# Performance work log

Measured on AMD Instinct MI355X. Metric: run time of the kernel, lower is better.

Reference implementation:

```python
import jax, jax.numpy as jnp
import numpy as np

COST_CLASS = 1.0
COST_MASK = 5.0
COST_DICE = 5.0


def _sample_points(masks, coords):
    """Bilinear grid_sample (align_corners=False, zero padding).

    masks:  [N, H, W] float
    coords: [P, 2] in [0, 1], (x, y) order as in torch grid_sample
    returns [N, P]
    """
    H, W = masks.shape[-2], masks.shape[-1]
    # torch: grid = 2*c - 1; pixel = ((grid+1)*size - 1)/2 = c*size - 0.5
    x = coords[:, 0] * W - 0.5
    y = coords[:, 1] * H - 0.5
    x0 = jnp.floor(x)
    y0 = jnp.floor(y)
    tx = (x - x0).astype(masks.dtype)
    ty = (y - y0).astype(masks.dtype)
    x0i = x0.astype(jnp.int32)
    y0i = y0.astype(jnp.int32)

    def gather(ix, iy):
        valid = ((ix >= 0) & (ix < W) & (iy >= 0) & (iy < H)).astype(masks.dtype)
        v = masks[:, jnp.clip(iy, 0, H - 1), jnp.clip(ix, 0, W - 1)]  # [N, P]
        return v * valid

    v00 = gather(x0i, y0i)
    v01 = gather(x0i + 1, y0i)
    v10 = gather(x0i, y0i + 1)
    v11 = gather(x0i + 1, y0i + 1)
    return (v00 * (1 - tx) * (1 - ty) + v01 * tx * (1 - ty)
            + v10 * (1 - tx) * ty + v11 * tx * ty)


def _cost_one(pred_mask, pred_logits, tgt_mask, labels, coords):
    # pred_mask [Q,H,W], pred_logits [Q,C], tgt_mask [T,H,W], labels [T], coords [P,2]
    probs = jax.nn.softmax(pred_logits, axis=-1)          # [Q, C]
    cost_class = -probs[:, labels]                        # [Q, T]

    pm = _sample_points(pred_mask, coords)                # [Q, P] logits
    tm = _sample_points(tgt_mask, coords)                 # [T, P] in [0,1]
    P = pm.shape[1]

    # pair-wise sigmoid BCE: BCE(x, 1) = softplus(-x), BCE(x, 0) = softplus(x)
    ce_pos = jax.nn.softplus(-pm) / P                     # [Q, P]
    ce_neg = jax.nn.softplus(pm) / P                      # [Q, P]
    cost_mask = ce_pos @ tm.T + ce_neg @ (1.0 - tm).T     # [Q, T]

    # pair-wise dice
    sig = jax.nn.sigmoid(pm)                              # [Q, P]
    numerator = 2.0 * (sig @ tm.T)                        # [Q, T]
    denominator = sig.sum(-1)[:, None] + tm.sum(-1)[None, :]
    cost_dice = 1.0 - (numerator + 1.0) / (denominator + 1.0)

    return COST_MASK * cost_mask + COST_CLASS * cost_class + COST_DICE * cost_dice


def setup_inputs() -> dict:
    key = jax.random.key(0)
    k1, k2, k3, k4, k5 = jax.random.split(key, 5)
    B, Q, C, T, H, W, P = 8, 150, 134, 32, 160, 160, 12544
    masks_queries_logits = jax.random.normal(k1, (B, Q, H, W), dtype=jnp.float32)
    class_queries_logits = jax.random.normal(k2, (B, Q, C), dtype=jnp.float32)
    # binary target masks
    mask_labels = (jax.random.uniform(k3, (B, T, H, W)) > 0.5).astype(jnp.float32)
    class_labels = jax.random.randint(k4, (B, T), 0, 133, dtype=jnp.int64)
    point_coords = jax.random.uniform(k5, (B, P, 2), dtype=jnp.float32)
    return {
        "masks_queries_logits": masks_queries_logits,
        "class_queries_logits": class_queries_logits,
        "mask_labels": mask_labels,
        "class_labels": class_labels,
        "point_coords": point_coords,
    }


def reference(masks_queries_logits, class_queries_logits, mask_labels, class_labels, point_coords):
    # Returns the per-sample cost matrices [B, Q, T] (the GPU-side work of the
    # matcher). The scipy Hungarian assignment on these matrices is CPU-bound
    # and intentionally excluded from the kernel baseline.
    cost = jax.vmap(_cost_one)(
        masks_queries_logits, class_queries_logits, mask_labels, class_labels, point_coords
    )
    return cost
```

## Files before the change

### kernel.cpp

```cpp
#include <hip/hip_runtime.h>
#include <hip/hip_bf16.h>
#include <hip/hip_fp16.h>
#include <math.h>

#define B_ 8
#define Q_ 150
#define QP_ 160
#define C_ 134
#define T_ 32
#define H_ 160
#define W_ 160
#define P_ 12544
#define HW_ (H_ * W_)
#define HW4_ (HW_ / 4)

#define SBLK 1024
#define SFULL 12
#define STAIL 256
#define SEG_ 28
#define KSEG 448
#define KITER 14
#define DSTRIDE (2 * B_ * QP_ * T_)

typedef __attribute__((ext_vector_type(8))) short short8;
typedef __attribute__((ext_vector_type(4))) float floatx4;

struct Samp {
  int i00, i01, i10, i11;
  float w00, w01, w10, w11;
};

__device__ __forceinline__ Samp make_samp(float cx, float cy) {
  float x = cx * (float)W_ - 0.5f;
  float y = cy * (float)H_ - 0.5f;
  float x0f = floorf(x), y0f = floorf(y);
  float tx = x - x0f, ty = y - y0f;
  int x0 = (int)x0f, y0 = (int)y0f;
  int x1 = x0 + 1, y1 = y0 + 1;
  bool vx0 = (x0 >= 0) && (x0 < W_);
  bool vx1 = (x1 >= 0) && (x1 < W_);
  bool vy0 = (y0 >= 0) && (y0 < H_);
  bool vy1 = (y1 >= 0) && (y1 < H_);
  int cx0 = min(max(x0, 0), W_ - 1), cx1 = min(max(x1, 0), W_ - 1);
  int cy0 = min(max(y0, 0), H_ - 1), cy1 = min(max(y1, 0), H_ - 1);
  Samp s;
  s.i00 = cy0 * W_ + cx0;
  s.i01 = cy0 * W_ + cx1;
  s.i10 = cy1 * W_ + cx0;
  s.i11 = cy1 * W_ + cx1;
  float w00 = (1.f - tx) * (1.f - ty);
  float w01 = tx * (1.f - ty);
  float w10 = (1.f - tx) * ty;
  float w11 = tx * ty;
  s.w00 = (vx0 && vy0) ? w00 : 0.f;
  s.w01 = (vx1 && vy0) ? w01 : 0.f;
  s.w10 = (vx0 && vy1) ? w10 : 0.f;
  s.w11 = (vx1 && vy1) ? w11 : 0.f;
  return s;
}

__device__ __forceinline__ float waveSum(float v) {
#pragma unroll
  for (int m = 32; m >= 1; m >>= 1) v += __shfl_xor(v, m, 64);
  return v;
}
__device__ __forceinline__ float waveMax(float v) {
#pragma unroll
  for (int m = 32; m >= 1; m >>= 1) v = fmaxf(v, __shfl_xor(v, m, 64));
  return v;
}

__device__ __forceinline__ unsigned short f2bf(float x) {
  union { __hip_bfloat16 h; unsigned short u; } cv;
  cv.h = __float2bfloat16(x);
  return cv.u;
}
__device__ __forceinline__ float bf2f(unsigned short u) {
  return __uint_as_float(((unsigned int)u) << 16);
}
__device__ __forceinline__ float h2f(unsigned short u) {
  union { __half h; unsigned short u; } cv;
  cv.u = u;
  return __half2float(cv.h);
}
__device__ __forceinline__ unsigned short f2h(float x) {
  union { __half h; unsigned short u; } cv;
  cv.h = __float2half(x);
  return cv.u;
}

__launch_bounds__(256) __global__
void samp_kernel(const float* __restrict__ coords,
                 unsigned int* __restrict__ sIdx,
                 uint2* __restrict__ sW) {
  int i = blockIdx.x * 256 + threadIdx.x;
  float2 cc = ((const float2*)coords)[i];
  Samp s = make_samp(cc.x, cc.y);
  int dx = s.i01 - s.i00;
  int dy = (s.i10 != s.i00) ? 1 : 0;
  sIdx[i] = (unsigned)s.i00 | ((unsigned)dx << 15) | ((unsigned)dy << 16);
  uint2 w;
  w.x = (unsigned)f2h(s.w00) | ((unsigned)f2h(s.w01) << 16);
  w.y = (unsigned)f2h(s.w10) | ((unsigned)f2h(s.w11) << 16);
  sW[i] = w;
}

__device__ __forceinline__ float lds_sample(const unsigned short* img,
                                            unsigned iv, uint2 wv) {
  int i00 = iv & 0x7fff;
  int i01 = i00 + ((iv >> 15) & 1);
  int ir = (iv & 0x10000) ? W_ : 0;
  return h2f(wv.x & 0xffff) * bf2f(img[i00]) +
         h2f(wv.x >> 16) * bf2f(img[i01]) +
         h2f(wv.y & 0xffff) * bf2f(img[i00 + ir]) +
         h2f(wv.y >> 16) * bf2f(img[i01 + ir]);
}

__launch_bounds__(SBLK) __global__
void sample_kernel(const float* __restrict__ masks_q,
                   const float* __restrict__ mask_labels,
                   const unsigned int* __restrict__ sIdx,
                   const uint2* __restrict__ sW,
                   unsigned short* __restrict__ pmh,
                   unsigned short* __restrict__ tmh,
                   float* __restrict__ S_sp, float* __restrict__ S_sig,
                   float* __restrict__ S_tm) {
  __shared__ unsigned short img[HW_];
  __shared__ float red[32];
  const int x = blockIdx.x;
  const int b = blockIdx.y;
  const int tid = threadIdx.x;
  const bool isPm = (x < Q_);

  const float* src = isPm ? (masks_q + ((size_t)b * Q_ + x) * HW_)
                          : (mask_labels + ((size_t)b * T_ + (x - Q_)) * HW_);
  const float4* s4 = (const float4*)src;
  for (int i = tid; i < HW4_; i += SBLK) {
    float4 v = s4[i];
    ushort4 u;
    u.x = f2bf(v.x); u.y = f2bf(v.y); u.z = f2bf(v.z); u.w = f2bf(v.w);
    *(ushort4*)&img[4 * i] = u;
  }
  __syncthreads();

  const unsigned int* sIdxB = sIdx + (size_t)b * P_;
  const uint2* sWB = sW + (size_t)b * P_;

  if (isPm) {
    unsigned short* dst = pmh + ((size_t)b * QP_ + x) * P_;
    float ssp = 0.f, ssg = 0.f;
#pragma unroll 2
    for (int c = 0; c < SFULL; ++c) {
      int p = c * SBLK + tid;
      float pm = lds_sample(img, sIdxB[p], sWB[p]);
      float e = __expf(-fabsf(pm));
      float sp = fmaxf(pm, 0.f) + __logf(1.f + e);
      float r = __builtin_amdgcn_rcpf(1.f + e);
      float sg = (pm >= 0.f) ? r : e * r;
      ssp += sp;
      ssg += sg;
      dst[p] = f2bf(pm);
    }
    if (tid < STAIL) {
      int p = SFULL * SBLK + tid;
      float pm = lds_sample(img, sIdxB[p], sWB[p]);
      float e = __expf(-fabsf(pm));
      float sp = fmaxf(pm, 0.f) + __logf(1.f + e);
      float r = __builtin_amdgcn_rcpf(1.f + e);
      float sg = (pm >= 0.f) ? r : e * r;
      ssp += sp;
      ssg += sg;
      dst[p] = f2bf(pm);
    }
    ssp = waveSum(ssp);
    ssg = waveSum(ssg);
    int w = tid >> 6;
    if ((tid & 63) == 0) {
      red[w] = ssp;
      red[16 + w] = ssg;
    }
    __syncthreads();
    if (tid == 0) {
      float a = 0.f, bb = 0.f;
#pragma unroll
      for (int i = 0; i < 16; ++i) { a += red[i]; bb += red[16 + i]; }
      S_sp[b * Q_ + x] = a;
      S_sig[b * Q_ + x] = bb;
    }
  } else {
    const int t = x - Q_;
    unsigned short* dst = tmh + ((size_t)b * T_ + t) * P_;
    float stm = 0.f;
#pragma unroll 2
    for (int c = 0; c < SFULL; ++c) {
      int p = c * SBLK + tid;
      float v = lds_sample(img, sIdxB[p], sWB[p]);
      stm += v;
      dst[p] = f2bf(v);
    }
    if (tid < STAIL) {
      int p = SFULL * SBLK + tid;
      float v = lds_sample(img, sIdxB[p], sWB[p]);
      stm += v;
      dst[p] = f2bf(v);
    }
    stm = waveSum(stm);
    int w = tid >> 6;
    if ((tid & 63) == 0) red[w] = stm;
    __syncthreads();
    if (tid == 0) {
      float a = 0.f;
#pragma unroll
      for (int i = 0; i < 16; ++i) a += red[i];
      S_tm[b * T_ + t] = a;
    }
  }
}

__device__ __forceinline__ short8 sig_frag(short8 a) {
  short8 out;
#pragma unroll
  for (int j = 0; j < 8; ++j) {
    float x = bf2f((unsigned short)a[j]);
    float e = __expf(-fabsf(x));
    float r = __builtin_amdgcn_rcpf(1.f + e);
    float sg = (x >= 0.f) ? r : e * r;
    out[j] = (short)f2bf(sg);
  }
  return out;
}

__launch_bounds__(320) __global__
void gemm_kernel(const unsigned short* __restrict__ pmh,
                 const unsigned short* __restrict__ tmh,
                 float* __restrict__ accP) {
  const int b = blockIdx.y;
  const int seg = blockIdx.x;
  const int w = threadIdx.x >> 6;
  const int l = threadIdx.x & 63;
  const int quad = l >> 4;
  const int mrow = l & 15;

  const unsigned short* pmb = pmh + ((size_t)b * QP_ + w * 32) * P_;
  const unsigned short* tmb = tmh + (size_t)b * T_ * P_;

  floatx4 aL[2][2];
  floatx4 aS[2][2];
#pragma unroll
  for (int i = 0; i < 2; ++i)
#pragma unroll
    for (int j = 0; j < 2; ++j) {
      aL[i][j] = (floatx4){0.f, 0.f, 0.f, 0.f};
      aS[i][j] = (floatx4){0.f, 0.f, 0.f, 0.f};
    }

  const int kbase = seg * KSEG;
#pragma unroll 2
  for (int ki = 0; ki < KITER; ++ki) {
    const int k0 = kbase + ki * 32 + quad * 8;
    short8 a0 = *(const short8*)(pmb + (size_t)(0 * 16 + mrow) * P_ + k0);
    short8 a1 = *(const short8*)(pmb + (size_t)(1 * 16 + mrow) * P_ + k0);
    short8 b0 = *(const short8*)(tmb + (size_t)(0 * 16 + mrow) * P_ + k0);
    short8 b1 = *(const short8*)(tmb + (size_t)(1 * 16 + mrow) * P_ + k0);
    short8 s0 = sig_frag(a0);
    short8 s1 = sig_frag(a1);
    aL[0][0] = __builtin_amdgcn_mfma_f32_16x16x32_bf16(a0, b0, aL[0][0], 0, 0, 0);
    aL[0][1] = __builtin_amdgcn_mfma_f32_16x16x32_bf16(a0, b1, aL[0][1], 0, 0, 0);
    aL[1][0] = __builtin_amdgcn_mfma_f32_16x16x32_bf16(a1, b0, aL[1][0], 0, 0, 0);
    aL[1][1] = __builtin_amdgcn_mfma_f32_16x16x32_bf16(a1, b1, aL[1][1], 0, 0, 0);
    aS[0][0] = __builtin_amdgcn_mfma_f32_16x16x32_bf16(s0, b0, aS[0][0], 0, 0, 0);
    aS[0][1] = __builtin_amdgcn_mfma_f32_16x16x32_bf16(s0, b1, aS[0][1], 0, 0, 0);
    aS[1][0] = __builtin_amdgcn_mfma_f32_16x16x32_bf16(s1, b0, aS[1][0], 0, 0, 0);
    aS[1][1] = __builtin_amdgcn_mfma_f32_16x16x32_bf16(s1, b1, aS[1][1], 0, 0, 0);
  }

  float* base = accP + (size_t)seg * DSTRIDE;
#pragma unroll
  for (int mtl = 0; mtl < 2; ++mtl)
#pragma unroll
    for (int nt = 0; nt < 2; ++nt)
#pragma unroll
      for (int r = 0; r < 4; ++r) {
        int q = w * 32 + mtl * 16 + quad * 4 + r;
        int t = nt * 16 + mrow;
        base[((size_t)(0 * B_ + b) * QP_ + q) * T_ + t] = aL[mtl][nt][r];
        base[((size_t)(1 * B_ + b) * QP_ + q) * T_ + t] = aS[mtl][nt][r];
      }
}

__launch_bounds__(256) __global__
void reduce_kernel(const float* __restrict__ accP, float* __restrict__ accD) {
  int i = blockIdx.x * 256 + threadIdx.x;
  float s = 0.f;
#pragma unroll
  for (int seg = 0; seg < SEG_; ++seg) s += accP[(size_t)seg * DSTRIDE + i];
  accD[i] = s;
}

__launch_bounds__(64) __global__
void final_kernel(const float* __restrict__ class_q,
                  const int* __restrict__ labels,
                  const float* __restrict__ accD,
                  const float* __restrict__ S_sp,
                  const float* __restrict__ S_sig,
                  const float* __restrict__ S_tm,
                  float* __restrict__ out) {
  const int bq = blockIdx.x;
  const int b = bq / Q_;
  const int q = bq % Q_;
  const int l = threadIdx.x;
  const float* cl = class_q + (size_t)bq * C_;

  float v = -INFINITY;
  for (int c = l; c < C_; c += 64) v = fmaxf(v, cl[c]);
  float m = waveMax(v);
  float e = 0.f;
  for (int c = l; c < C_; c += 64) e += __expf(cl[c] - m);
  float den = waveSum(e);

  if (l < T_) {
    int t = l;
    int lbl = labels[b * T_ + t];
    float prob = __expf(cl[lbl] - m) / den;
    float Dlin = accD[((size_t)(0 * B_ + b) * QP_ + q) * T_ + t];
    float Dsig = accD[((size_t)(1 * B_ + b) * QP_ + q) * T_ + t];
    float cmask = (S_sp[bq] - Dlin) * (1.f / (float)P_);
    float dice = 1.f - (2.f * Dsig + 1.f) / (S_sig[bq] + S_tm[b * T_ + t] + 1.f);
    out[(size_t)bq * T_ + t] = 5.f * cmask + 5.f * dice - prob;
  }
}

extern "C" void kernel_launch(void* const* d_in, const int* in_sizes, int n_in,
                              void* d_out, int out_size, void* d_ws,
                              size_t ws_size, hipStream_t stream) {
  const float* masks_q = (const float*)d_in[0];
  const float* class_q = (const float*)d_in[1];
  const float* mask_labels = (const float*)d_in[2];
  const int* class_labels = (const int*)d_in[3];
  const float* coords = (const float*)d_in[4];
  float* out = (float*)d_out;

  float* accD = (float*)d_ws;
  float* accP = accD + DSTRIDE;
  uint2* sW = (uint2*)(accP + (size_t)SEG_ * DSTRIDE);
  unsigned int* sIdx = (unsigned int*)(sW + (size_t)B_ * P_);
  float* S_sp = (float*)(sIdx + (size_t)B_ * P_);
  float* S_sig = S_sp + B_ * Q_;
  float* S_tm = S_sig + B_ * Q_;
  unsigned short* pmh = (unsigned short*)(S_tm + B_ * T_);
  unsigned short* tmh = pmh + (size_t)B_ * QP_ * P_;

  samp_kernel<<<(B_ * P_) / 256, 256, 0, stream>>>(coords, sIdx, sW);
  sample_kernel<<<dim3(Q_ + T_, B_), SBLK, 0, stream>>>(
      masks_q, mask_labels, sIdx, sW, pmh, tmh, S_sp, S_sig, S_tm);
  gemm_kernel<<<dim3(SEG_, B_), 320, 0, stream>>>(pmh, tmh, accP);
  reduce_kernel<<<DSTRIDE / 256, 256, 0, stream>>>(accP, accD);
  final_kernel<<<B_ * Q_, 64, 0, stream>>>(class_q, class_labels, accD, S_sp,
                                           S_sig, S_tm, out);
}
```

Measured before the change: 244.7 us.

## Batch sampling loads, rewrite softplus via rcp, and split GEMM K finer

```diff
diff --git a/kernel.cpp b/kernel.cpp
--- a/kernel.cpp
+++ b/kernel.cpp
@@ -15,11 +15,11 @@
 #define HW4_ (HW_ / 4)
 
 #define SBLK 1024
-#define SFULL 12
+#define SBATCH 3
 #define STAIL 256
-#define SEG_ 28
-#define KSEG 448
-#define KITER 14
+#define SEG_ 56
+#define KSEG 224
+#define KITER 7
 #define DSTRIDE (2 * B_ * QP_ * T_)
 
 typedef __attribute__((ext_vector_type(8))) short short8;
@@ -116,7 +116,7 @@
          h2f(wv.y >> 16) * bf2f(img[i01 + ir]);
 }
 
-__launch_bounds__(SBLK) __global__
+__launch_bounds__(SBLK, 8) __global__
 void sample_kernel(const float* __restrict__ masks_q,
                    const float* __restrict__ mask_labels,
                    const unsigned int* __restrict__ sIdx,
@@ -135,12 +135,21 @@
   const float* src = isPm ? (masks_q + ((size_t)b * Q_ + x) * HW_)
                           : (mask_labels + ((size_t)b * T_ + (x - Q_)) * HW_);
   const float4* s4 = (const float4*)src;
-  for (int i = tid; i < HW4_; i += SBLK) {
+#pragma unroll
+  for (int c = 0; c < 6; ++c) {
+    int i = c * SBLK + tid;
     float4 v = s4[i];
     ushort4 u;
     u.x = f2bf(v.x); u.y = f2bf(v.y); u.z = f2bf(v.z); u.w = f2bf(v.w);
     *(ushort4*)&img[4 * i] = u;
   }
+  if (tid < HW4_ - 6 * SBLK) {
+    int i = 6 * SBLK + tid;
+    float4 v = s4[i];
+    ushort4 u;
+    u.x = f2bf(v.x); u.y = f2bf(v.y); u.z = f2bf(v.z); u.w = f2bf(v.w);
+    *(ushort4*)&img[4 * i] = u;
+  }
   __syncthreads();
 
   const unsigned int* sIdxB = sIdx + (size_t)b * P_;
@@ -149,24 +158,36 @@
   if (isPm) {
     unsigned short* dst = pmh + ((size_t)b * QP_ + x) * P_;
     float ssp = 0.f, ssg = 0.f;
-#pragma unroll 2
-    for (int c = 0; c < SFULL; ++c) {
-      int p = c * SBLK + tid;
+    for (int c = 0; c < SBATCH; ++c) {
+      int p = c * (4 * SBLK) + tid;
+      unsigned iv[4];
+      uint2 wv[4];
+      float v[4];
+#pragma unroll
+      for (int j = 0; j < 4; ++j) {
+        iv[j] = sIdxB[p + j * SBLK];
+        wv[j] = sWB[p + j * SBLK];
+      }
+#pragma unroll
+      for (int j = 0; j < 4; ++j) v[j] = lds_sample(img, iv[j], wv[j]);
+#pragma unroll
+      for (int j = 0; j < 4; ++j) {
+        float pm = v[j];
+        float e = __expf(-fabsf(pm));
+        float r = __builtin_amdgcn_rcpf(1.f + e);
+        float sp = fmaxf(pm, 0.f) - __logf(r);
+        float sg = (pm >= 0.f) ? r : e * r;
+        ssp += sp;
+        ssg += sg;
+        dst[p + j * SBLK] = f2bf(pm);
+      }
+    }
+    if (tid < STAIL) {
+      int p = SBATCH * 4 * SBLK + tid;
       float pm = lds_sample(img, sIdxB[p], sWB[p]);
       float e = __expf(-fabsf(pm));
-      float sp = fmaxf(pm, 0.f) + __logf(1.f + e);
       float r = __builtin_amdgcn_rcpf(1.f + e);
-      float sg = (pm >= 0.f) ? r : e * r;
-      ssp += sp;
-      ssg += sg;
-      dst[p] = f2bf(pm);
-    }
-    if (tid < STAIL) {
-      int p = SFULL * SBLK + tid;
-      float pm = lds_sample(img, sIdxB[p], sWB[p]);
-      float e = __expf(-fabsf(pm));
-      float sp = fmaxf(pm, 0.f) + __logf(1.f + e);
-      float r = __builtin_amdgcn_rcpf(1.f + e);
+      float sp = fmaxf(pm, 0.f) - __logf(r);
       float sg = (pm >= 0.f) ? r : e * r;
       ssp += sp;
       ssg += sg;
@@ -191,15 +212,24 @@
     const int t = x - Q_;
     unsigned short* dst = tmh + ((size_t)b * T_ + t) * P_;
     float stm = 0.f;
-#pragma unroll 2
-    for (int c = 0; c < SFULL; ++c) {
-      int p = c * SBLK + tid;
-      float v = lds_sample(img, sIdxB[p], sWB[p]);
-      stm += v;
-      dst[p] = f2bf(v);
+    for (int c = 0; c < SBATCH; ++c) {
+      int p = c * (4 * SBLK) + tid;
+      unsigned iv[4];
+      uint2 wv[4];
+#pragma unroll
+      for (int j = 0; j < 4; ++j) {
+        iv[j] = sIdxB[p + j * SBLK];
+        wv[j] = sWB[p + j * SBLK];
+      }
+#pragma unroll
+      for (int j = 0; j < 4; ++j) {
+        float v = lds_sample(img, iv[j], wv[j]);
+        stm += v;
+        dst[p + j * SBLK] = f2bf(v);
+      }
     }
     if (tid < STAIL) {
-      int p = SFULL * SBLK + tid;
+      int p = SBATCH * 4 * SBLK + tid;
       float v = lds_sample(img, sIdxB[p], sWB[p]);
       stm += v;
       dst[p] = f2bf(v);
@@ -255,7 +285,7 @@
     }
 
   const int kbase = seg * KSEG;
-#pragma unroll 2
+#pragma unroll
   for (int ki = 0; ki < KITER; ++ki) {
     const int k0 = kbase + ki * 32 + quad * 8;
     short8 a0 = *(const short8*)(pmb + (size_t)(0 * 16 + mrow) * P_ + k0);
```

Result: no change. 240.7 us (-1.6%).
